# Optimization experiments

Measured on AMD Instinct MI355X. Metric: run time of the kernel, lower is better.

## Reference

```python
import jax, jax.numpy as jnp
import numpy as np

N = 100000      # nodes
E = 1600000     # edges
D_IN, H1, H2, D_OUT = 128, 64, 64, 64


def setup_inputs() -> dict:
    key = jax.random.key(0)
    ks = jax.random.split(key, 9)
    x = jax.random.normal(ks[0], (N, D_IN), dtype=jnp.float32)
    edge_index = jax.random.randint(ks[1], (2, E), 0, N, dtype=jnp.int32)
    def lin(k, fan_in, fan_out):
        s = 1.0 / np.sqrt(fan_in)
        return jax.random.uniform(k, (fan_in, fan_out), jnp.float32, -s, s)
    W1 = lin(ks[2], D_IN, H1); b1 = jnp.zeros((H1,), jnp.float32)
    W2 = lin(ks[3], H1, H2);  b2 = jnp.zeros((H2,), jnp.float32)
    W3 = lin(ks[4], H2, D_OUT); b3 = jnp.zeros((D_OUT,), jnp.float32)
    return {"x": x, "W1": W1, "b1": b1, "W2": W2, "b2": b2,
            "W3": W3, "b3": b3, "edge_index": edge_index}


def reference(x, W1, b1, W2, b2, W3, b3, edge_index):
    src, dst = edge_index[0], edge_index[1]
    # GCN symmetric normalization with self-loops: deg = in-degree + 1
    deg = jnp.zeros((N,), x.dtype).at[dst].add(1.0) + 1.0
    dinv = jax.lax.rsqrt(deg)                 # [N]
    norm = dinv[src] * dinv[dst]              # [E] edge weights
    self_norm = dinv * dinv                   # [N] self-loop weights

    def conv(h, W, b):
        h = h @ W                             # transform first (PyG GCNConv)
        msg = h[src] * norm[:, None]          # [E, F] gathered messages
        agg = jnp.zeros_like(h).at[dst].add(msg) + self_norm[:, None] * h
        return agg + b

    h = jax.nn.relu(conv(x, W1, b1))          # dropout is identity in eval
    h = jax.nn.relu(conv(h, W2, b2))
    return conv(h, W3, b3)
```

## Files before the change

### kernel.cpp

```cpp
#include <hip/hip_runtime.h>
#include <hip/hip_bf16.h>

#define D_IN 128
#define F 64
#define R_EDGES 4096

__global__ __launch_bounds__(256) void part1_kernel(
        const int* __restrict__ src, const int* __restrict__ dst, int E,
        unsigned long long M37, int cap1, uint2* __restrict__ ebufB,
        int* __restrict__ bcur1) {
    __shared__ int wcnt[64], incl64[64], cur[64], gbase[16];
    const int t = threadIdx.x, w = t >> 6, lane = t & 63;
    const int base = blockIdx.x * R_EDGES;
    const int lim = min(base + R_EDGES, E);

    if (t < 64) wcnt[t] = 0;
    __syncthreads();

    for (int i = base + t; i < lim; i += 256) {
        int d = dst[i];
        int b = (int)(((unsigned long long)(unsigned)d * M37) >> 37) >> 4;
        atomicAdd(&wcnt[b * 4 + w], 1);
    }
    __syncthreads();

    if (t < 64) {
        int v = wcnt[t], x = v;
        for (int dlt = 1; dlt < 64; dlt <<= 1) { int y = __shfl_up(x, dlt); if (lane >= dlt) x += y; }
        incl64[t] = x;
        wcnt[t] = x - v;
    }
    __syncthreads();
    if (t < 16) {
        int T = incl64[t * 4 + 3] - (t ? incl64[t * 4 - 1] : 0);
        gbase[t] = T > 0 ? atomicAdd(&bcur1[t], T) : 0;
    }
    __syncthreads();
    if (t < 64) cur[t] = gbase[t >> 2] + wcnt[t] - wcnt[(t >> 2) << 2];
    __syncthreads();

    for (int i = base + t; i < lim; i += 256) {
        int s = src[i], d = dst[i];
        int b = (int)(((unsigned long long)(unsigned)d * M37) >> 37) >> 4;
        int p = atomicAdd(&cur[b * 4 + w], 1);
        ebufB[(size_t)b * cap1 + p] = make_uint2((unsigned)s, (unsigned)d);
    }
}

#define BPB2 27
__global__ __launch_bounds__(256) void part2_kernel(
        const uint2* __restrict__ ebufB, const int* __restrict__ bcur1,
        unsigned long long M37, int cap1, int cap2,
        uint2* __restrict__ ebufA, int* __restrict__ bcur2) {
    __shared__ int wcnt[64], incl64[64], cur[64], gbase[16];
    const int t = threadIdx.x, w = t >> 6, lane = t & 63;
    const int b1 = blockIdx.x / BPB2, r = blockIdx.x % BPB2;
    const int cnt1 = bcur1[b1];
    const int beg = r * R_EDGES, lim = min(beg + R_EDGES, cnt1);
    if (beg >= cnt1) return;
    const uint2* in = ebufB + (size_t)b1 * cap1;

    if (t < 64) wcnt[t] = 0;
    __syncthreads();

    for (int i = beg + t; i < lim; i += 256) {
        unsigned d = in[i].y;
        int b = (int)(((unsigned long long)d * M37) >> 37) & 15;
        atomicAdd(&wcnt[b * 4 + w], 1);
    }
    __syncthreads();

    if (t < 64) {
        int v = wcnt[t], x = v;
        for (int dlt = 1; dlt < 64; dlt <<= 1) { int y = __shfl_up(x, dlt); if (lane >= dlt) x += y; }
        incl64[t] = x;
        wcnt[t] = x - v;
    }
    __syncthreads();
    if (t < 16) {
        int T = incl64[t * 4 + 3] - (t ? incl64[t * 4 - 1] : 0);
        gbase[t] = T > 0 ? atomicAdd(&bcur2[b1 * 16 + t], T) : 0;
    }
    __syncthreads();
    if (t < 64) cur[t] = gbase[t >> 2] + wcnt[t] - wcnt[(t >> 2) << 2];
    __syncthreads();

    for (int i = beg + t; i < lim; i += 256) {
        uint2 e = in[i];
        int b = (int)(((unsigned long long)e.y * M37) >> 37) & 15;
        int p = atomicAdd(&cur[b * 4 + w], 1);
        ebufA[(size_t)(b1 * 16 + b) * cap2 + p] = e;
    }
}

__global__ __launch_bounds__(256) void scan256_kernel(const int* __restrict__ bcur2,
                                                      int* __restrict__ bbase,
                                                      int* __restrict__ offsets, int n, int E) {
    __shared__ int tmp[256];
    int t = threadIdx.x;
    int v = bcur2[t];
    tmp[t] = v;
    __syncthreads();
    for (int off = 1; off < 256; off <<= 1) {
        int a = (t >= off) ? tmp[t - off] : 0;
        __syncthreads();
        if (t >= off) tmp[t] += a;
        __syncthreads();
    }
    bbase[t] = tmp[t] - v;
    if (t == 0) offsets[n] = E;
}

__global__ __launch_bounds__(256) void bsort_kernel(
        const uint2* __restrict__ ebufA, const int* __restrict__ bcur2,
        const int* __restrict__ bbase, int cap2, int NPB, int n,
        int* __restrict__ csr, int* __restrict__ offsets, float* __restrict__ dinv) {
    __shared__ int cnt[512], excl[512];
    const int sb = blockIdx.x, t = threadIdx.x;
    const int node0 = sb * NPB;
    const int nn = min(NPB, n - node0);
    if (nn <= 0) return;
    const int cE = bcur2[sb];
    const int base = bbase[sb];
    const uint2* eb = ebufA + (size_t)sb * cap2;

    for (int i = t; i < 512; i += 256) cnt[i] = 0;
    __syncthreads();
    for (int i = t; i < cE; i += 256) atomicAdd(&cnt[eb[i].y - node0], 1);
    __syncthreads();

    if (t < 64) {
        int carry = 0;
        for (int c = 0; c < 8; ++c) {
            int v = cnt[c * 64 + t], x = v;
            for (int dlt = 1; dlt < 64; dlt <<= 1) { int y = __shfl_up(x, dlt); if (t >= dlt) x += y; }
            excl[c * 64 + t] = carry + x - v;
            carry += __shfl(x, 63);
        }
    }
    __syncthreads();

    for (int i = t; i < nn; i += 256) {
        offsets[node0 + i] = base + excl[i];
        dinv[node0 + i] = rsqrtf((float)cnt[i] + 1.0f);
    }
    __syncthreads();
    for (int i = t; i < 512; i += 256) cnt[i] = excl[i];
    __syncthreads();
    for (int i = t; i < cE; i += 256) {
        uint2 e = eb[i];
        int p = atomicAdd(&cnt[e.y - node0], 1);
        csr[base + p] = (int)e.x;
    }
}

template<int K, bool RELU_IN>
__global__ __launch_bounds__(256) void gemm_kernel(
        const float* __restrict__ A, const float* __restrict__ W,
        const float* __restrict__ dinv, float* __restrict__ h2, int n) {
    constexpr int F4 = K / 4;
    __shared__ float4 Al[64 * F4];
    __shared__ float  Wl[K * F];
    const int t = threadIdx.x;

    for (int i = t; i < K * F / 4; i += 256)
        ((float4*)Wl)[i] = ((const float4*)W)[i];

    const int row0 = blockIdx.x * 64;
    for (int i = t; i < 64 * F4; i += 256) {
        int r = i / F4, k4 = i % F4;
        int gr = row0 + r; if (gr >= n) gr = n - 1;
        float4 v = ((const float4*)(A + (size_t)gr * K))[k4];
        if (RELU_IN) {
            v.x = fmaxf(v.x, 0.f); v.y = fmaxf(v.y, 0.f);
            v.z = fmaxf(v.z, 0.f); v.w = fmaxf(v.w, 0.f);
        }
        Al[r * F4 + (k4 ^ ((r >> 2) & 7))] = v;
    }
    __syncthreads();

    const int rg = t >> 4, cg = t & 15;
    const int r0 = rg * 4, c0 = cg * 4;
    const int sw = rg & 7;

    float acc[4][4] = {};
#pragma unroll 2
    for (int k4 = 0; k4 < F4; ++k4) {
        float4 a[4];
#pragma unroll
        for (int i = 0; i < 4; ++i) a[i] = Al[(r0 + i) * F4 + (k4 ^ sw)];
#pragma unroll
        for (int j = 0; j < 4; ++j) {
            float4 w = *(const float4*)&Wl[(k4 * 4 + j) * F + c0];
#pragma unroll
            for (int i = 0; i < 4; ++i) {
                float av = (j == 0) ? a[i].x : (j == 1) ? a[i].y : (j == 2) ? a[i].z : a[i].w;
                acc[i][0] = fmaf(av, w.x, acc[i][0]);
                acc[i][1] = fmaf(av, w.y, acc[i][1]);
                acc[i][2] = fmaf(av, w.z, acc[i][2]);
                acc[i][3] = fmaf(av, w.w, acc[i][3]);
            }
        }
    }

#pragma unroll
    for (int i = 0; i < 4; ++i) {
        int gr = row0 + r0 + i;
        if (gr < n) {
            float dv = dinv[gr];
            float4 o = make_float4(acc[i][0] * dv, acc[i][1] * dv,
                                   acc[i][2] * dv, acc[i][3] * dv);
            *(float4*)&h2[(size_t)gr * F + c0] = o;
        }
    }
}

__global__ __launch_bounds__(256) void agg_kernel(
        const int* __restrict__ offsets, const int* __restrict__ csr,
        const float* __restrict__ dinv, const float* __restrict__ h2,
        const float* __restrict__ bvec, float* __restrict__ out, int n) {
    const int wid  = (int)((blockIdx.x * 256u + threadIdx.x) >> 6);
    const int lane = threadIdx.x & 63;
    const int g = lane >> 3, q8 = lane & 7;
    if (wid >= n) return;
    const size_t fo = (size_t)q8 * 8;

    const int beg = offsets[wid], end = offsets[wid + 1];

    float4 a00 = {0,0,0,0}, a01 = {0,0,0,0};
    float4 a10 = {0,0,0,0}, a11 = {0,0,0,0};
    if (g == 0) {
        a00 = *(const float4*)&h2[(size_t)wid * F + fo];
        a01 = *(const float4*)&h2[(size_t)wid * F + fo + 4];
    }

    int j = beg + g;
    for (; j + 8 < end; j += 16) {
        int s0 = csr[j], s1 = csr[j + 8];
        const float* r0 = &h2[(size_t)s0 * F + fo];
        const float* r1 = &h2[(size_t)s1 * F + fo];
        float4 v00 = *(const float4*)r0;
        float4 v01 = *(const float4*)(r0 + 4);
        float4 v10 = *(const float4*)r1;
        float4 v11 = *(const float4*)(r1 + 4);
        a00.x += v00.x; a00.y += v00.y; a00.z += v00.z; a00.w += v00.w;
        a01.x += v01.x; a01.y += v01.y; a01.z += v01.z; a01.w += v01.w;
        a10.x += v10.x; a10.y += v10.y; a10.z += v10.z; a10.w += v10.w;
        a11.x += v11.x; a11.y += v11.y; a11.z += v11.z; a11.w += v11.w;
    }
    if (j < end) {
        int s0 = csr[j];
        const float* r0 = &h2[(size_t)s0 * F + fo];
        float4 v00 = *(const float4*)r0;
        float4 v01 = *(const float4*)(r0 + 4);
        a00.x += v00.x; a00.y += v00.y; a00.z += v00.z; a00.w += v00.w;
        a01.x += v01.x; a01.y += v01.y; a01.z += v01.z; a01.w += v01.w;
    }
    a00.x += a10.x; a00.y += a10.y; a00.z += a10.z; a00.w += a10.w;
    a01.x += a11.x; a01.y += a11.y; a01.z += a11.z; a01.w += a11.w;

#pragma unroll
    for (int m = 8; m < 64; m <<= 1) {
        a00.x += __shfl_xor(a00.x, m); a00.y += __shfl_xor(a00.y, m);
        a00.z += __shfl_xor(a00.z, m); a00.w += __shfl_xor(a00.w, m);
        a01.x += __shfl_xor(a01.x, m); a01.y += __shfl_xor(a01.y, m);
        a01.z += __shfl_xor(a01.z, m); a01.w += __shfl_xor(a01.w, m);
    }

    if (g == 0) {
        float dv = dinv[wid];
        float4 b0 = *(const float4*)&bvec[fo];
        float4 b1 = *(const float4*)&bvec[fo + 4];
        float4 o0 = make_float4(fmaf(dv, a00.x, b0.x), fmaf(dv, a00.y, b0.y),
                                fmaf(dv, a00.z, b0.z), fmaf(dv, a00.w, b0.w));
        float4 o1 = make_float4(fmaf(dv, a01.x, b1.x), fmaf(dv, a01.y, b1.y),
                                fmaf(dv, a01.z, b1.z), fmaf(dv, a01.w, b1.w));
        *(float4*)&out[(size_t)wid * F + fo] = o0;
        *(float4*)&out[(size_t)wid * F + fo + 4] = o1;
    }
}

extern "C" void kernel_launch(void* const* d_in, const int* in_sizes, int n_in,
                              void* d_out, int out_size, void* d_ws, size_t ws_size,
                              hipStream_t stream) {
    const float* x   = (const float*)d_in[0];
    const float* W1  = (const float*)d_in[1];
    const float* b1  = (const float*)d_in[2];
    const float* W2  = (const float*)d_in[3];
    const float* b2  = (const float*)d_in[4];
    const float* W3  = (const float*)d_in[5];
    const float* b3  = (const float*)d_in[6];
    const int*   ei  = (const int*)d_in[7];

    const int n = in_sizes[0] / D_IN;
    const int E = in_sizes[7] / 2;
    const int* src = ei;
    const int* dst = ei + E;

    const int NPB = (n + 255) >> 8;
    const unsigned long long M37 = ((1ull << 37) / (unsigned long long)NPB) + 1;
    const int cap1 = E / 16 + 4096;
    const int cap2 = 8192;

    char* p = (char*)d_ws;
    auto alloc = [&](size_t bytes) { char* q = p; p += (bytes + 255) & ~(size_t)255; return q; };
    int*   bcur1   = (int*)  alloc((16 + 256) * 4);
    int*   bcur2   = bcur1 + 16;
    int*   bbase   = (int*)  alloc(256 * 4);
    int*   offsets = (int*)  alloc((size_t)(n + 1) * 4);
    float* dinv    = (float*)alloc((size_t)n * 4);
    int*   csr     = (int*)  alloc((size_t)E * 4);
    float* h2      = (float*)alloc((size_t)n * F * 4);
    float* outA    = (float*)alloc((size_t)n * F * 4);
    float* outF    = (float*)d_out;

    uint2* ebufB = (uint2*)h2;
    uint2* ebufA = (uint2*)outA;

    const int p1Blocks = (E + R_EDGES - 1) / R_EDGES;
    const int gBlocks  = (n + 63) / 64;
    const int aBlocks  = (int)(((size_t)n * 64 + 255) / 256);

    hipMemsetAsync(bcur1, 0, (16 + 256) * 4, stream);
    part1_kernel <<<p1Blocks,  256, 0, stream>>>(src, dst, E, M37, cap1, ebufB, bcur1);
    part2_kernel <<<16 * BPB2, 256, 0, stream>>>(ebufB, bcur1, M37, cap1, cap2, ebufA, bcur2);
    scan256_kernel<<<1,        256, 0, stream>>>(bcur2, bbase, offsets, n, E);
    bsort_kernel <<<256,       256, 0, stream>>>(ebufA, bcur2, bbase, cap2, NPB, n,
                                                 csr, offsets, dinv);

    gemm_kernel<D_IN, false><<<gBlocks, 256, 0, stream>>>(x, W1, dinv, h2, n);
    agg_kernel<<<aBlocks, 256, 0, stream>>>(offsets, csr, dinv, h2, b1, outA, n);

    gemm_kernel<F, true><<<gBlocks, 256, 0, stream>>>(outA, W2, dinv, h2, n);
    agg_kernel<<<aBlocks, 256, 0, stream>>>(offsets, csr, dinv, h2, b2, outA, n);

    gemm_kernel<F, true><<<gBlocks, 256, 0, stream>>>(outA, W3, dinv, h2, n);
    agg_kernel<<<aBlocks, 256, 0, stream>>>(offsets, csr, dinv, h2, b3, outF, n);
}
```

Measured before the change: 311.6 us.

## Replace two-pass edge bucketing with single 256-way partition pass

Collapses the two-level radix partition (16 then 16 sub-buckets) into one kernel that scatters edges directly into 256 destination buckets. The separate 256-entry scan kernel is folded into the bucket-sort kernel, where each block recomputes the bucket base scan. This removes one full read and write of the edge buffer and two kernel launches. In exchange the scatter writes go to 256 destinations per block, so they are less coalesced and contend on more shared-memory and global atomics.

```diff
diff --git a/kernel.cpp b/kernel.cpp
--- a/kernel.cpp
+++ b/kernel.cpp
@@ -5,123 +5,63 @@
 #define F 64
 #define R_EDGES 4096
 
-__global__ __launch_bounds__(256) void part1_kernel(
+__global__ __launch_bounds__(256) void part256_kernel(
         const int* __restrict__ src, const int* __restrict__ dst, int E,
-        unsigned long long M37, int cap1, uint2* __restrict__ ebufB,
-        int* __restrict__ bcur1) {
-    __shared__ int wcnt[64], incl64[64], cur[64], gbase[16];
-    const int t = threadIdx.x, w = t >> 6, lane = t & 63;
+        unsigned long long M37, int cap2,
+        uint2* __restrict__ ebufA, int* __restrict__ bcur2) {
+    __shared__ int cnt[256], gb[256];
+    const int t = threadIdx.x;
     const int base = blockIdx.x * R_EDGES;
     const int lim = min(base + R_EDGES, E);
 
-    if (t < 64) wcnt[t] = 0;
+    cnt[t] = 0;
     __syncthreads();
 
     for (int i = base + t; i < lim; i += 256) {
-        int d = dst[i];
-        int b = (int)(((unsigned long long)(unsigned)d * M37) >> 37) >> 4;
-        atomicAdd(&wcnt[b * 4 + w], 1);
-    }
-    __syncthreads();
-
-    if (t < 64) {
-        int v = wcnt[t], x = v;
-        for (int dlt = 1; dlt < 64; dlt <<= 1) { int y = __shfl_up(x, dlt); if (lane >= dlt) x += y; }
-        incl64[t] = x;
-        wcnt[t] = x - v;
-    }
-    __syncthreads();
-    if (t < 16) {
-        int T = incl64[t * 4 + 3] - (t ? incl64[t * 4 - 1] : 0);
-        gbase[t] = T > 0 ? atomicAdd(&bcur1[t], T) : 0;
-    }
-    __syncthreads();
-    if (t < 64) cur[t] = gbase[t >> 2] + wcnt[t] - wcnt[(t >> 2) << 2];
+        int b = (int)(((unsigned long long)(unsigned)dst[i] * M37) >> 37);
+        atomicAdd(&cnt[b], 1);
+    }
+    __syncthreads();
+
+    int c = cnt[t];
+    gb[t] = (c > 0) ? atomicAdd(&bcur2[t], c) : 0;
+    cnt[t] = 0;
     __syncthreads();
 
     for (int i = base + t; i < lim; i += 256) {
         int s = src[i], d = dst[i];
-        int b = (int)(((unsigned long long)(unsigned)d * M37) >> 37) >> 4;
-        int p = atomicAdd(&cur[b * 4 + w], 1);
-        ebufB[(size_t)b * cap1 + p] = make_uint2((unsigned)s, (unsigned)d);
-    }
-}
-
-#define BPB2 27
-__global__ __launch_bounds__(256) void part2_kernel(
-        const uint2* __restrict__ ebufB, const int* __restrict__ bcur1,
-        unsigned long long M37, int cap1, int cap2,
-        uint2* __restrict__ ebufA, int* __restrict__ bcur2) {
-    __shared__ int wcnt[64], incl64[64], cur[64], gbase[16];
-    const int t = threadIdx.x, w = t >> 6, lane = t & 63;
-    const int b1 = blockIdx.x / BPB2, r = blockIdx.x % BPB2;
-    const int cnt1 = bcur1[b1];
-    const int beg = r * R_EDGES, lim = min(beg + R_EDGES, cnt1);
-    if (beg >= cnt1) return;
-    const uint2* in = ebufB + (size_t)b1 * cap1;
-
-    if (t < 64) wcnt[t] = 0;
-    __syncthreads();
-
-    for (int i = beg + t; i < lim; i += 256) {
-        unsigned d = in[i].y;
-        int b = (int)(((unsigned long long)d * M37) >> 37) & 15;
-        atomicAdd(&wcnt[b * 4 + w], 1);
-    }
-    __syncthreads();
-
-    if (t < 64) {
-        int v = wcnt[t], x = v;
-        for (int dlt = 1; dlt < 64; dlt <<= 1) { int y = __shfl_up(x, dlt); if (lane >= dlt) x += y; }
-        incl64[t] = x;
-        wcnt[t] = x - v;
-    }
-    __syncthreads();
-    if (t < 16) {
-        int T = incl64[t * 4 + 3] - (t ? incl64[t * 4 - 1] : 0);
-        gbase[t] = T > 0 ? atomicAdd(&bcur2[b1 * 16 + t], T) : 0;
-    }
-    __syncthreads();
-    if (t < 64) cur[t] = gbase[t >> 2] + wcnt[t] - wcnt[(t >> 2) << 2];
-    __syncthreads();
-
-    for (int i = beg + t; i < lim; i += 256) {
-        uint2 e = in[i];
-        int b = (int)(((unsigned long long)e.y * M37) >> 37) & 15;
-        int p = atomicAdd(&cur[b * 4 + w], 1);
-        ebufA[(size_t)(b1 * 16 + b) * cap2 + p] = e;
-    }
-}
-
-__global__ __launch_bounds__(256) void scan256_kernel(const int* __restrict__ bcur2,
-                                                      int* __restrict__ bbase,
-                                                      int* __restrict__ offsets, int n, int E) {
-    __shared__ int tmp[256];
-    int t = threadIdx.x;
-    int v = bcur2[t];
-    tmp[t] = v;
-    __syncthreads();
-    for (int off = 1; off < 256; off <<= 1) {
-        int a = (t >= off) ? tmp[t - off] : 0;
-        __syncthreads();
-        if (t >= off) tmp[t] += a;
-        __syncthreads();
-    }
-    bbase[t] = tmp[t] - v;
-    if (t == 0) offsets[n] = E;
+        int b = (int)(((unsigned long long)(unsigned)d * M37) >> 37);
+        int p = atomicAdd(&cnt[b], 1);
+        ebufA[(size_t)b * cap2 + gb[b] + p] = make_uint2((unsigned)s, (unsigned)d);
+    }
 }
 
 __global__ __launch_bounds__(256) void bsort_kernel(
         const uint2* __restrict__ ebufA, const int* __restrict__ bcur2,
-        const int* __restrict__ bbase, int cap2, int NPB, int n,
+        int cap2, int NPB, int n, int E,
         int* __restrict__ csr, int* __restrict__ offsets, float* __restrict__ dinv) {
-    __shared__ int cnt[512], excl[512];
+    __shared__ int cnt[512], excl[512], bb[256];
     const int sb = blockIdx.x, t = threadIdx.x;
     const int node0 = sb * NPB;
     const int nn = min(NPB, n - node0);
+
+    bb[t] = bcur2[t];
+    __syncthreads();
+    if (t < 64) {
+        int carry = 0;
+        for (int c4 = 0; c4 < 4; ++c4) {
+            int v = bb[c4 * 64 + t], x = v;
+            for (int dlt = 1; dlt < 64; dlt <<= 1) { int y = __shfl_up(x, dlt); if (t >= dlt) x += y; }
+            bb[c4 * 64 + t] = carry + x - v;
+            carry += __shfl(x, 63);
+        }
+    }
+    __syncthreads();
+
+    if (sb == 255 && t == 0) offsets[n] = E;
     if (nn <= 0) return;
     const int cE = bcur2[sb];
-    const int base = bbase[sb];
+    const int base = bb[sb];
     const uint2* eb = ebufA + (size_t)sb * cap2;
 
     for (int i = t; i < 512; i += 256) cnt[i] = 0;
@@ -131,10 +71,10 @@
 
     if (t < 64) {
         int carry = 0;
-        for (int c = 0; c < 8; ++c) {
-            int v = cnt[c * 64 + t], x = v;
+        for (int c4 = 0; c4 < 8; ++c4) {
+            int v = cnt[c4 * 64 + t], x = v;
             for (int dlt = 1; dlt < 64; dlt <<= 1) { int y = __shfl_up(x, dlt); if (t >= dlt) x += y; }
-            excl[c * 64 + t] = carry + x - v;
+            excl[c4 * 64 + t] = carry + x - v;
             carry += __shfl(x, 63);
         }
     }
@@ -299,14 +239,11 @@
 
     const int NPB = (n + 255) >> 8;
     const unsigned long long M37 = ((1ull << 37) / (unsigned long long)NPB) + 1;
-    const int cap1 = E / 16 + 4096;
     const int cap2 = 8192;
 
     char* p = (char*)d_ws;
     auto alloc = [&](size_t bytes) { char* q = p; p += (bytes + 255) & ~(size_t)255; return q; };
-    int*   bcur1   = (int*)  alloc((16 + 256) * 4);
-    int*   bcur2   = bcur1 + 16;
-    int*   bbase   = (int*)  alloc(256 * 4);
+    int*   bcur2   = (int*)  alloc(256 * 4);
     int*   offsets = (int*)  alloc((size_t)(n + 1) * 4);
     float* dinv    = (float*)alloc((size_t)n * 4);
     int*   csr     = (int*)  alloc((size_t)E * 4);
@@ -314,19 +251,16 @@
     float* outA    = (float*)alloc((size_t)n * F * 4);
     float* outF    = (float*)d_out;
 
-    uint2* ebufB = (uint2*)h2;
     uint2* ebufA = (uint2*)outA;
 
-    const int p1Blocks = (E + R_EDGES - 1) / R_EDGES;
-    const int gBlocks  = (n + 63) / 64;
-    const int aBlocks  = (int)(((size_t)n * 64 + 255) / 256);
-
-    hipMemsetAsync(bcur1, 0, (16 + 256) * 4, stream);
-    part1_kernel <<<p1Blocks,  256, 0, stream>>>(src, dst, E, M37, cap1, ebufB, bcur1);
-    part2_kernel <<<16 * BPB2, 256, 0, stream>>>(ebufB, bcur1, M37, cap1, cap2, ebufA, bcur2);
-    scan256_kernel<<<1,        256, 0, stream>>>(bcur2, bbase, offsets, n, E);
-    bsort_kernel <<<256,       256, 0, stream>>>(ebufA, bcur2, bbase, cap2, NPB, n,
-                                                 csr, offsets, dinv);
+    const int pBlocks = (E + R_EDGES - 1) / R_EDGES;
+    const int gBlocks = (n + 63) / 64;
+    const int aBlocks = (int)(((size_t)n * 64 + 255) / 256);
+
+    hipMemsetAsync(bcur2, 0, 256 * 4, stream);
+    part256_kernel<<<pBlocks, 256, 0, stream>>>(src, dst, E, M37, cap2, ebufA, bcur2);
+    bsort_kernel  <<<256,     256, 0, stream>>>(ebufA, bcur2, cap2, NPB, n, E,
+                                                csr, offsets, dinv);
 
     gemm_kernel<D_IN, false><<<gBlocks, 256, 0, stream>>>(x, W1, dinv, h2, n);
     agg_kernel<<<aBlocks, 256, 0, stream>>>(offsets, csr, dinv, h2, b1, outA, n);
```

Result: faster. 302.2 us (-3.0%).
